# Optimization experiments

Hardware: AMD Instinct MI355X
Metric: run time of the kernel (lower is better)

The kernel has to match this reference:

```python
import jax, jax.numpy as jnp
import numpy as np

N_NODES = 50000
N_EDGES = 800000
C_FEAT = 96
HID = 96
C_CONST = 0.005


def _psi(v):
    return jnp.sign(v) * jnp.log(jnp.abs(v) + 1.0)


def setup_inputs() -> dict:
    key = jax.random.key(0)
    ks = jax.random.split(key, 16)
    d_e_in = 2 * C_FEAT + 2
    d_h_in = 2 * C_FEAT
    def w(k, fan_in, fan_out):
        return jax.random.normal(k, (fan_in, fan_out), jnp.float32) * (1.0 / np.sqrt(fan_in))
    return {
        "x": jax.random.normal(ks[0], (N_NODES, 4), jnp.float32),
        "h": jax.random.normal(ks[1], (N_NODES, C_FEAT), jnp.float32),
        "edge_i": jax.random.randint(ks[2], (N_EDGES,), 0, N_NODES, jnp.int32),
        "edge_j": jax.random.randint(ks[3], (N_EDGES,), 0, N_NODES, jnp.int32),
        "We1": w(ks[4], d_e_in, HID), "be1": jnp.zeros((HID,), jnp.float32),
        "We2": w(ks[5], HID, HID), "be2": jnp.zeros((HID,), jnp.float32),
        "Wm": w(ks[6], HID, 1), "bm": jnp.zeros((1,), jnp.float32),
        "Wh1": w(ks[7], d_h_in, HID), "bh1": jnp.zeros((HID,), jnp.float32),
        "Wh2": w(ks[8], HID, C_FEAT), "bh2": jnp.zeros((C_FEAT,), jnp.float32),
        "Wx1": w(ks[9], HID, HID), "bx1": jnp.zeros((HID,), jnp.float32),
        "Wx2": w(ks[10], HID, 1),  # bias-free last phi_x layer
    }


def reference(x, h, edge_i, edge_j, We1, be1, We2, be2, Wm, bm,
              Wh1, bh1, Wh2, bh2, Wx1, bx1, Wx2):
    n = x.shape[0]
    x_i = x[edge_i]            # (K,4)
    x_j = x[edge_j]            # (K,4)
    # Minkowski invariants: 2*t-component - full Euclidean sum == (+,-,-,-)
    d2 = jnp.square(x_i - x_j)
    norms = 2.0 * d2[..., 0] - jnp.sum(d2, axis=-1)
    z = x_i * x_j
    prods = 2.0 * z[..., 0] - jnp.sum(z, axis=-1)
    norms = _psi(norms)[:, None]   # (K,1)
    prods = _psi(prods)[:, None]   # (K,1)

    e_in = jnp.concatenate([h[edge_i], h[edge_j], norms, prods], axis=-1)  # (K,2C+2)
    m = jax.nn.relu(jax.nn.relu(e_in @ We1 + be1) @ We2 + be2)             # (K,HID)
    w_gate = jax.nn.sigmoid(m @ Wm + bm)                                   # (K,1)

    wm = jax.ops.segment_sum(w_gate * m, edge_i, num_segments=n)          # (N,HID)
    dh = jax.nn.relu(jnp.concatenate([h, wm], axis=-1) @ Wh1 + bh1) @ Wh2 + bh2
    h_out = h + dh

    phi_x = jax.nn.relu(m @ Wx1 + bx1) @ Wx2                              # (K,1)
    vals = phi_x * x_j                                                     # (K,4)
    s = jax.ops.segment_sum(vals, edge_i, num_segments=n)                 # (N,4)
    cnt = jax.ops.segment_sum(jnp.ones((vals.shape[0],), vals.dtype), edge_i, num_segments=n)
    mean = jnp.where(cnt[:, None] > 0, s / jnp.maximum(cnt[:, None], 1.0), 0.0)
    x_out = x + C_CONST * mean
    return (h_out, x_out)
```

## Files before the change

kernel.cpp:

```cpp
#include <hip/hip_runtime.h>
#include <math.h>

#define NN 50000
#define NE 800000
#define NB 196
#define TE 128

typedef __attribute__((ext_vector_type(8))) short short8v;
typedef __attribute__((ext_vector_type(4))) float f32x4;

__device__ __forceinline__ int rfl(int v) { return __builtin_amdgcn_readfirstlane(v); }
__device__ __forceinline__ unsigned short f2bf(float f) {
  unsigned u = __float_as_uint(f);
  u += 0x7FFFu + ((u >> 16) & 1u);
  return (unsigned short)(u >> 16);
}
__device__ __forceinline__ unsigned pk2(float a, float b) {
  return (unsigned)f2bf(a) | ((unsigned)f2bf(b) << 16);
}
__device__ __forceinline__ float bflo(unsigned u) { return __uint_as_float(u << 16); }
__device__ __forceinline__ float bfhi(unsigned u) { return __uint_as_float(u & 0xFFFF0000u); }

__global__ void khist(const int* __restrict__ ei, int* __restrict__ cnt) {
  const int i = blockIdx.x * 256 + threadIdx.x;
  atomicAdd(&cnt[ei[i]], 1);
}

__global__ void kscanA(const int* __restrict__ cnt, int* __restrict__ pre,
                       int* __restrict__ bsum) {
  __shared__ int ps[256];
  const int b = blockIdx.x, t = threadIdx.x, idx = b * 256 + t;
  const int v = (idx < NN) ? cnt[idx] : 0;
  ps[t] = v;
  __syncthreads();
  for (int off = 1; off < 256; off <<= 1) {
    const int u = (t >= off) ? ps[t - off] : 0;
    __syncthreads();
    ps[t] += u;
    __syncthreads();
  }
  if (idx < NN) pre[idx] = ps[t] - v;
  if (t == 255) bsum[b] = ps[255];
}

__global__ void kscanB(const int* __restrict__ bsum, int* __restrict__ boff) {
  __shared__ int ps[256];
  const int t = threadIdx.x;
  const int v = (t < NB) ? bsum[t] : 0;
  ps[t] = v;
  __syncthreads();
  for (int off = 1; off < 256; off <<= 1) {
    const int u = (t >= off) ? ps[t - off] : 0;
    __syncthreads();
    ps[t] += u;
    __syncthreads();
  }
  if (t < NB) boff[t] = ps[t] - v;
}

__global__ void kscanC(const int* __restrict__ pre, const int* __restrict__ boff,
                       int* __restrict__ base, int* __restrict__ cursor) {
  const int b = blockIdx.x, t = threadIdx.x, idx = b * 256 + t;
  if (idx < NN) {
    const int v = pre[idx] + boff[b];
    base[idx] = v;
    cursor[idx] = v;
  }
  if (idx == 0) base[NN] = NE;
}

__global__ void kperm(const int* __restrict__ ei, const int* __restrict__ ej,
                      int* __restrict__ cursor,
                      int* __restrict__ eis, int* __restrict__ ejs) {
  const int i = blockIdx.x * 256 + threadIdx.x;
  const int vi = ei[i];
  const int pos = atomicAdd(&cursor[vi], 1);
  eis[pos] = vi;
  ejs[pos] = ej[i];
}

__global__ void kwprep(const float* __restrict__ We1, const float* __restrict__ We2,
                       const float* __restrict__ Wx1, const float* __restrict__ Wh1,
                       const float* __restrict__ Wh2,
                       unsigned short* __restrict__ We1p, unsigned short* __restrict__ We2p,
                       unsigned short* __restrict__ Wx1p, unsigned short* __restrict__ Wh1p,
                       unsigned short* __restrict__ Wh2p) {
  const int t = blockIdx.x * 256 + threadIdx.x;
  const int j = t & 7, lane = (t >> 3) & 63;
  const int kk = (lane >> 4) * 8 + j;
  const int nn = lane & 15;
  {
    const int tile = t >> 9, tk = tile / 12, tn = tile % 12;
    const int k = tk * 32 + kk, n2 = tn * 16 + nn;
    const float v = (n2 < 96) ? We1[k * 96 + n2] : We1[(96 + k) * 96 + (n2 - 96)];
    We1p[t] = f2bf(v);
  }
  {
    const int tile = t >> 9, tk = tile / 6, tn = tile % 6;
    const int k = tk * 32 + kk, n = tn * 16 + nn;
    Wh1p[t] = f2bf(Wh1[k * 96 + n]);
  }
  if (t < 9216) {
    const int tile = t >> 9, tk = tile / 6, tn = tile % 6;
    const int k = tk * 32 + kk, n = tn * 16 + nn;
    We2p[t] = f2bf(We2[k * 96 + n]);
    Wx1p[t] = f2bf(Wx1[k * 96 + n]);
    Wh2p[t] = f2bf(Wh2[k * 96 + n]);
  }
}

__global__ __launch_bounds__(256, 4) void k0_AB(const float* __restrict__ h,
                                                const unsigned short* __restrict__ We1p,
                                                unsigned short* __restrict__ Abf,
                                                unsigned short* __restrict__ Bbf) {
  __shared__ __align__(16) unsigned short hbT[64 * 104];
  __shared__ __align__(16) unsigned short outT[64 * 200];
  const int tid = threadIdx.x;
  const int nb = blockIdx.x * 64;
  {
    const int e = tid & 63, q = tid >> 6;
    const int node = nb + e;
    const int nc = node < NN ? node : NN - 1;
    const float* hr = h + (long)nc * 96 + q * 24;
    unsigned* dst = (unsigned*)hbT + e * 52 + q * 12;
    #pragma unroll
    for (int c = 0; c < 6; ++c) {
      const float4 v = *(const float4*)(hr + c * 4);
      dst[c * 2]     = pk2(v.x, v.y);
      dst[c * 2 + 1] = pk2(v.z, v.w);
    }
  }
  __syncthreads();
  const int l = tid & 63, w = tid >> 6, cg = l & 15, rg = l >> 4;
  {
    const short8v* Wp = (const short8v*)We1p;
    const unsigned short* ar = hbT + (w * 16 + cg) * 104;
    const short8v af0 = *(const short8v*)(ar + rg * 8);
    const short8v af1 = *(const short8v*)(ar + 32 + rg * 8);
    const short8v af2 = *(const short8v*)(ar + 64 + rg * 8);
    #pragma unroll
    for (int tn = 0; tn < 12; ++tn) {
      f32x4 acc = (f32x4){0.f, 0.f, 0.f, 0.f};
      acc = __builtin_amdgcn_mfma_f32_16x16x32_bf16(af0, Wp[(0 * 12 + tn) * 64 + l], acc, 0, 0, 0);
      acc = __builtin_amdgcn_mfma_f32_16x16x32_bf16(af1, Wp[(1 * 12 + tn) * 64 + l], acc, 0, 0, 0);
      acc = __builtin_amdgcn_mfma_f32_16x16x32_bf16(af2, Wp[(2 * 12 + tn) * 64 + l], acc, 0, 0, 0);
      #pragma unroll
      for (int r = 0; r < 4; ++r)
        outT[(w * 16 + rg * 4 + r) * 200 + tn * 16 + cg] = f2bf(acc[r]);
    }
  }
  __syncthreads();
  {
    const int e = tid & 63, q = tid >> 6;
    const int node = nb + e;
    if (node < NN) {
      const unsigned* src = (const unsigned*)outT + e * 100;
      if (q < 2) {
        uint4* dA = (uint4*)(Abf + (size_t)node * 96);
        #pragma unroll
        for (int i = 0; i < 6; ++i) dA[q * 6 + i] = *(const uint4*)(src + (q * 6 + i) * 4);
      } else {
        uint4* dB = (uint4*)(Bbf + (size_t)node * 96);
        #pragma unroll
        for (int i = 0; i < 6; ++i) dB[(q - 2) * 6 + i] = *(const uint4*)(src + 48 + ((q - 2) * 6 + i) * 4);
      }
    }
  }
}

__global__ __launch_bounds__(256, 5) void k1_edge(const float* __restrict__ x,
    const unsigned short* __restrict__ Abf, const unsigned short* __restrict__ Bbf,
    const int* __restrict__ eis, const int* __restrict__ ejs,
    const float* __restrict__ We1, const float* __restrict__ be1,
    const unsigned short* __restrict__ We2p, const float* __restrict__ be2,
    const float* __restrict__ Wm, const float* __restrict__ bm,
    const unsigned short* __restrict__ Wx1p, const float* __restrict__ bx1,
    const float* __restrict__ Wx2,
    float* __restrict__ wmo, float* __restrict__ svo) {
  __shared__ __align__(16) unsigned short actT[TE * 104];
  __shared__ float gl[TE];
  __shared__ float phil[TE];
  __shared__ __align__(16) float xjl[TE * 4];
  __shared__ int vseq[TE + 2];
  __shared__ unsigned long long bmask[2];

  const int tid = threadIdx.x;
  const float bm0 = bm[0];
  const int tb = blockIdx.x * TE;

  {
    const int e2 = tid & 127, hf = tid >> 7;
    const int fb = hf * 48;
    const int vi = eis[tb + e2], vj = ejs[tb + e2];
    const float4 xi = *(const float4*)(x + (long)vi * 4);
    const float4 xj = *(const float4*)(x + (long)vj * 4);
    if (hf == 0) {
      vseq[1 + e2] = vi;
      *(float4*)(xjl + e2 * 4) = xj;
    }
    if (tid == 0) {
      vseq[0] = (tb > 0) ? eis[tb - 1] : -1;
      vseq[TE + 1] = (tb + TE < NE) ? eis[tb + TE] : -1;
    }
    const float d0 = xi.x - xj.x, d1 = xi.y - xj.y, d2 = xi.z - xj.z, d3 = xi.w - xj.w;
    const float nrm = d0 * d0 - d1 * d1 - d2 * d2 - d3 * d3;
    const float prd = xi.x * xj.x - xi.y * xj.y - xi.z * xj.z - xi.w * xj.w;
    const float pn = copysignf(logf(fabsf(nrm) + 1.f), nrm);
    const float pp = copysignf(logf(fabsf(prd) + 1.f), prd);
    const uint4* Ar = (const uint4*)(Abf + (size_t)vi * 96 + fb);
    const uint4* Br = (const uint4*)(Bbf + (size_t)vj * 96 + fb);
    const float* wA = We1 + 192 * 96 + fb;
    const float* wB = We1 + 193 * 96 + fb;
    const float* bE = be1 + fb;
    unsigned* arow = (unsigned*)actT + e2 * 52 + hf * 24;
    #pragma unroll
    for (int c = 0; c < 6; ++c) {
      const uint4 A4 = Ar[c], B4 = Br[c];
      const unsigned au[4] = {A4.x, A4.y, A4.z, A4.w};
      const unsigned bu[4] = {B4.x, B4.y, B4.z, B4.w};
      #pragma unroll
      for (int k2 = 0; k2 < 4; ++k2) {
        const int f = c * 8 + k2 * 2;
        const float lo = fmaxf(bflo(au[k2]) + bflo(bu[k2]) + pn * wA[f] + pp * wB[f] + bE[f], 0.f);
        const float hi = fmaxf(bfhi(au[k2]) + bfhi(bu[k2]) + pn * wA[f + 1] + pp * wB[f + 1] + bE[f + 1], 0.f);
        arow[c * 4 + k2] = pk2(lo, hi);
      }
    }
  }
  __syncthreads();

  if (tid < TE) {
    const int pred = (vseq[1 + tid] != vseq[2 + tid]) ? 1 : 0;
    const unsigned long long mk = __ballot(pred);
    if ((tid & 63) == 0) bmask[tid >> 6] = mk;
  }

  const int l = tid & 63, w = tid >> 6;
  const int cg = l & 15, rg = l >> 4;
  const int r0 = w * 32;
  const short8v* Wp2 = (const short8v*)We2p;
  const short8v* Wpx = (const short8v*)Wx1p;

  {
    short8v af[2][3];
    #pragma unroll
    for (int rt = 0; rt < 2; ++rt)
      #pragma unroll
      for (int tk = 0; tk < 3; ++tk)
        af[rt][tk] = *(const short8v*)(actT + (r0 + rt * 16 + cg) * 104 + tk * 32 + rg * 8);
    f32x4 acc[2][6];
    #pragma unroll
    for (int rt = 0; rt < 2; ++rt)
      #pragma unroll
      for (int tn = 0; tn < 6; ++tn) acc[rt][tn] = (f32x4){0.f, 0.f, 0.f, 0.f};
    #pragma unroll
    for (int tk = 0; tk < 3; ++tk)
      #pragma unroll
      for (int tn = 0; tn < 6; ++tn) {
        const short8v bf = Wp2[(tk * 6 + tn) * 64 + l];
        acc[0][tn] = __builtin_amdgcn_mfma_f32_16x16x32_bf16(af[0][tk], bf, acc[0][tn], 0, 0, 0);
        acc[1][tn] = __builtin_amdgcn_mfma_f32_16x16x32_bf16(af[1][tk], bf, acc[1][tn], 0, 0, 0);
      }
    #pragma unroll
    for (int rt = 0; rt < 2; ++rt) {
      float gp[4] = {0.f, 0.f, 0.f, 0.f};
      #pragma unroll
      for (int tn = 0; tn < 6; ++tn) {
        const int col = tn * 16 + cg;
        const float b = be2[col], wmw = Wm[col];
        #pragma unroll
        for (int r = 0; r < 4; ++r) {
          const float v = fmaxf(acc[rt][tn][r] + b, 0.f);
          gp[r] = fmaf(v, wmw, gp[r]);
          actT[(r0 + rt * 16 + rg * 4 + r) * 104 + col] = (unsigned short)f2bf(v);
        }
      }
      #pragma unroll
      for (int r = 0; r < 4; ++r) {
        float s = gp[r];
        s += __shfl_xor(s, 1); s += __shfl_xor(s, 2);
        s += __shfl_xor(s, 4); s += __shfl_xor(s, 8);
        if (cg == 0) gl[r0 + rt * 16 + rg * 4 + r] = 1.f / (1.f + expf(-(s + bm0)));
      }
    }
  }


  {
    short8v af[2][3];
    #pragma unroll
    for (int rt = 0; rt < 2; ++rt)
      #pragma unroll
      for (int tk = 0; tk < 3; ++tk)
        af[rt][tk] = *(const short8v*)(actT + (r0 + rt * 16 + cg) * 104 + tk * 32 + rg * 8);
    f32x4 acc[2][6];
    #pragma unroll
    for (int rt = 0; rt < 2; ++rt)
      #pragma unroll
      for (int tn = 0; tn < 6; ++tn) acc[rt][tn] = (f32x4){0.f, 0.f, 0.f, 0.f};
    #pragma unroll
    for (int tk = 0; tk < 3; ++tk)
      #pragma unroll
      for (int tn = 0; tn < 6; ++tn) {
        const short8v bf = Wpx[(tk * 6 + tn) * 64 + l];
        acc[0][tn] = __builtin_amdgcn_mfma_f32_16x16x32_bf16(af[0][tk], bf, acc[0][tn], 0, 0, 0);
        acc[1][tn] = __builtin_amdgcn_mfma_f32_16x16x32_bf16(af[1][tk], bf, acc[1][tn], 0, 0, 0);
      }
    #pragma unroll
    for (int rt = 0; rt < 2; ++rt) {
      float pp2[4] = {0.f, 0.f, 0.f, 0.f};
      #pragma unroll
      for (int tn = 0; tn < 6; ++tn) {
        const int col = tn * 16 + cg;
        const float b = bx1[col], wxw = Wx2[col];
        #pragma unroll
        for (int r = 0; r < 4; ++r)
          pp2[r] = fmaf(fmaxf(acc[rt][tn][r] + b, 0.f), wxw, pp2[r]);
      }
      #pragma unroll
      for (int r = 0; r < 4; ++r) {
        float s = pp2[r];
        s += __shfl_xor(s, 1); s += __shfl_xor(s, 2);
        s += __shfl_xor(s, 4); s += __shfl_xor(s, 8);
        if (cg == 0) phil[r0 + rt * 16 + rg * 4 + r] = s;
      }
    }
  }
  __syncthreads();

  if (tid < 192) {
    const int q0 = (tid >= 96) ? 1 : 0;
    const int col = tid - 96 * q0;
    #pragma unroll
    for (int pass = 0; pass < 2; ++pass) {
      const int q = q0 + 2 * pass;
      const int s_lo = q * 32;
      const unsigned long long mk = bmask[s_lo >> 6];
      float acc2 = 0.f;
      bool clean = (q == 0) ? (vseq[0] != vseq[1])
                            : (((bmask[(s_lo - 1) >> 6] >> ((s_lo - 1) & 63)) & 1ull) != 0);
      for (int i = 0; i < 32; ++i) {
        const int e = s_lo + i;
        acc2 = fmaf(gl[e], __uint_as_float(((unsigned)actT[e * 104 + col]) << 16), acc2);
        const bool gend = ((mk >> (e & 63)) & 1ull) != 0;
        if (gend || i == 31) {
          const int node = vseq[e + 1];
          float* dst = wmo + (size_t)node * 96 + col;
          if (clean && gend) *dst = acc2; else atomicAdd(dst, acc2);
          acc2 = 0.f; clean = true;
        }
      }
    }
  } else if (tid < 224) {
    const int t2 = tid - 192;
    const int comp = t2 & 3, q8 = t2 >> 2;
    const int s_lo = q8 * 16;
    const unsigned long long mk = bmask[s_lo >> 6];
    float acc2 = 0.f;
    bool clean = (q8 == 0) ? (vseq[0] != vseq[1])
                           : (((bmask[(s_lo - 1) >> 6] >> ((s_lo - 1) & 63)) & 1ull) != 0);
    for (int i = 0; i < 16; ++i) {
      const int e = s_lo + i;
      acc2 = fmaf(phil[e], xjl[e * 4 + comp], acc2);
      const bool gend = ((mk >> (e & 63)) & 1ull) != 0;
      if (gend || i == 15) {
        const int node = vseq[e + 1];
        float* dst = svo + (size_t)node * 4 + comp;
        if (clean && gend) *dst = acc2; else atomicAdd(dst, acc2);
        acc2 = 0.f; clean = true;
      }
    }
  }
}

__global__ __launch_bounds__(256, 4) void k3ab(const float* __restrict__ h,
    const float* __restrict__ wmv,
    const unsigned short* __restrict__ Wh1p, const float* __restrict__ bh1,
    const unsigned short* __restrict__ Wh2p, const float* __restrict__ bh2,
    const float* __restrict__ x, const float* __restrict__ svm,
    const int* __restrict__ basep,
    float* __restrict__ hout, float* __restrict__ xout) {
  __shared__ __align__(16) unsigned short inT[64 * 200];
  __shared__ __align__(16) unsigned short tmpT[64 * 104];
  const int tid = threadIdx.x;
  const int nb = blockIdx.x * 64;
  {
    const int e = tid & 63, q = tid >> 6;
    const int node = nb + e;
    const int nc = node < NN ? node : NN - 1;
    const float* hr = h + (long)nc * 96 + q * 24;
    const float* wr = wmv + (long)nc * 96 + q * 24;
    unsigned* dh = (unsigned*)inT + e * 100 + q * 12;
    unsigned* dw = (unsigned*)inT + e * 100 + 48 + q * 12;
    #pragma unroll
    for (int c = 0; c < 6; ++c) {
      const float4 v = *(const float4*)(hr + c * 4);
      dh[c * 2]     = pk2(v.x, v.y);
      dh[c * 2 + 1] = pk2(v.z, v.w);
      const float4 u = *(const float4*)(wr + c * 4);
      dw[c * 2]     = pk2(u.x, u.y);
      dw[c * 2 + 1] = pk2(u.z, u.w);
    }
  }
  __syncthreads();
  const int l = tid & 63, w = tid >> 6, cg = l & 15, rg = l >> 4;
  {
    const unsigned short* ar = inT + (w * 16 + cg) * 200;
    short8v af[6];
    #pragma unroll
    for (int tk = 0; tk < 6; ++tk) af[tk] = *(const short8v*)(ar + tk * 32 + rg * 8);
    const short8v* Wp = (const short8v*)Wh1p;
    #pragma unroll
    for (int tn = 0; tn < 6; ++tn) {
      f32x4 acc = (f32x4){0.f, 0.f, 0.f, 0.f};
      #pragma unroll
      for (int tk = 0; tk < 6; ++tk)
        acc = __builtin_amdgcn_mfma_f32_16x16x32_bf16(af[tk], Wp[(tk * 6 + tn) * 64 + l], acc, 0, 0, 0);
      const int col = tn * 16 + cg;
      const float b = bh1[col];
      #pragma unroll
      for (int r = 0; r < 4; ++r)
        tmpT[(w * 16 + rg * 4 + r) * 104 + col] = f2bf(fmaxf(acc[r] + b, 0.f));
    }
  }
  __syncthreads();
  {
    float* oT = (float*)inT;
    const unsigned short* mr = tmpT + (w * 16 + cg) * 104;
    const short8v mf0 = *(const short8v*)(mr + rg * 8);
    const short8v mf1 = *(const short8v*)(mr + 32 + rg * 8);
    const short8v mf2 = *(const short8v*)(mr + 64 + rg * 8);
    const short8v* Wp = (const short8v*)Wh2p;
    #pragma unroll
    for (int tn = 0; tn < 6; ++tn) {
      f32x4 acc = (f32x4){0.f, 0.f, 0.f, 0.f};
      acc = __builtin_amdgcn_mfma_f32_16x16x32_bf16(mf0, Wp[(0 * 6 + tn) * 64 + l], acc, 0, 0, 0);
      acc = __builtin_amdgcn_mfma_f32_16x16x32_bf16(mf1, Wp[(1 * 6 + tn) * 64 + l], acc, 0, 0, 0);
      acc = __builtin_amdgcn_mfma_f32_16x16x32_bf16(mf2, Wp[(2 * 6 + tn) * 64 + l], acc, 0, 0, 0);
      const int col = tn * 16 + cg;
      const float b = bh2[col];
      #pragma unroll
      for (int r = 0; r < 4; ++r)
        oT[(w * 16 + rg * 4 + r) * 100 + col] = acc[r] + b;
    }
  }
  __syncthreads();
  {
    const int e = tid & 63, q = tid >> 6;
    const int node = nb + e;
    if (node < NN) {
      const float* src = (const float*)inT + e * 100 + q * 24;
      const float* hr = h + (size_t)node * 96 + q * 24;
      float* dst = hout + (size_t)node * 96 + q * 24;
      #pragma unroll
      for (int c = 0; c < 6; ++c) {
        const float4 s = *(const float4*)(src + c * 4);
        const float4 hv = *(const float4*)(hr + c * 4);
        *(float4*)(dst + c * 4) = make_float4(hv.x + s.x, hv.y + s.y, hv.z + s.z, hv.w + s.w);
      }
    }
  }
  if (tid < 64) {
    const int node = nb + tid;
    if (node < NN) {
      const int cnt = basep[node + 1] - basep[node];
      const float inv = cnt > 0 ? 1.f / (float)cnt : 0.f;
      const float4 s4 = *(const float4*)(svm + (long)node * 4);
      const float4 xv = *(const float4*)(x + (long)node * 4);
      *(float4*)(xout + (long)node * 4) =
          make_float4(xv.x + 0.005f * s4.x * inv, xv.y + 0.005f * s4.y * inv,
                      xv.z + 0.005f * s4.z * inv, xv.w + 0.005f * s4.w * inv);
    }
  }
}

extern "C" void kernel_launch(void* const* d_in, const int* in_sizes, int n_in,
                              void* d_out, int out_size, void* d_ws, size_t ws_size,
                              hipStream_t stream) {
  const float* x   = (const float*)d_in[0];
  const float* h   = (const float*)d_in[1];
  const int*   ei  = (const int*)d_in[2];
  const int*   ej  = (const int*)d_in[3];
  const float* We1 = (const float*)d_in[4];
  const float* be1 = (const float*)d_in[5];
  const float* We2 = (const float*)d_in[6];
  const float* be2 = (const float*)d_in[7];
  const float* Wm  = (const float*)d_in[8];
  const float* bm  = (const float*)d_in[9];
  const float* Wh1 = (const float*)d_in[10];
  const float* bh1 = (const float*)d_in[11];
  const float* Wh2 = (const float*)d_in[12];
  const float* bh2 = (const float*)d_in[13];
  const float* Wx1 = (const float*)d_in[14];
  const float* bx1 = (const float*)d_in[15];
  const float* Wx2 = (const float*)d_in[16];

  char* w = (char*)d_ws;
  unsigned short* Abf  = (unsigned short*)w;
  unsigned short* Bbf  = (unsigned short*)(w + 9600000);
  float* WMv  = (float*)(w + 19200000);
  float* SvM  = (float*)(w + 38400000);
  int*   cnt  = (int*)(w + 39200000);
  int*   base = (int*)(w + 39400000);
  int*   curs = (int*)(w + 39600064);
  unsigned short* We2p = (unsigned short*)(w + 39800064);
  unsigned short* Wx1p = (unsigned short*)(w + 39818496);
  unsigned short* We1p = (unsigned short*)(w + 39836928);
  unsigned short* Wh1p = (unsigned short*)(w + 39873792);
  unsigned short* Wh2p = (unsigned short*)(w + 39910656);
  int*   eis  = (int*)(w + 39929088);
  int*   ejs  = (int*)(w + 43129088);
  int*   pre  = (int*)(w + 46329088);
  int*   bsum = (int*)(w + 46529088);
  int*   boff = (int*)(w + 46529872);

  float* hout = (float*)d_out;
  float* xout = hout + 4800000;

  hipMemsetAsync(cnt, 0, NN * sizeof(int), stream);
  hipMemsetAsync(WMv, 0, (size_t)(4800000 + 200000) * sizeof(float), stream);
  khist<<<NE / 256, 256, 0, stream>>>(ei, cnt);
  kscanA<<<NB, 256, 0, stream>>>(cnt, pre, bsum);
  kscanB<<<1, 256, 0, stream>>>(bsum, boff);
  kscanC<<<NB, 256, 0, stream>>>(pre, boff, base, curs);
  kperm<<<NE / 256, 256, 0, stream>>>(ei, ej, curs, eis, ejs);
  kwprep<<<72, 256, 0, stream>>>(We1, We2, Wx1, Wh1, Wh2, We1p, We2p, Wx1p, Wh1p, Wh2p);
  k0_AB<<<782, 256, 0, stream>>>(h, We1p, Abf, Bbf);
  k1_edge<<<NE / TE, 256, 0, stream>>>(x, Abf, Bbf, eis, ejs, We1, be1, We2p, be2,
                                       Wm, bm, Wx1p, bx1, Wx2, WMv, SvM);
  k3ab<<<782, 256, 0, stream>>>(h, WMv, Wh1p, bh1, Wh2p, bh2, x, SvM, base, hout, xout);
}
```

Baseline: 312.7 us.

## Fuse histogram with weight prep, load MFMA operands directly, tweak edge scatter

Merges the edge histogram and weight-packing kernels into one launch. k0_AB and k3ab now load h and wm straight from global memory into MFMA A-fragments instead of staging them through shared memory, which removes a barrier and LDS traffic and lets k0_AB raise its occupancy hint. It also adds s_setprio around MFMA loops, changes the activation LDS stride from 104 to 100, and rewrites the segmented scatter to walk whole segments using ctz on the boundary mask. The stride of 100 and the direct global loads may cause LDS bank conflicts or uncoalesced reads.

```diff
diff --git a/kernel.cpp b/kernel.cpp
--- a/kernel.cpp
+++ b/kernel.cpp
@@ -5,11 +5,11 @@
 #define NE 800000
 #define NB 196
 #define TE 128
+#define AST 100
 
 typedef __attribute__((ext_vector_type(8))) short short8v;
 typedef __attribute__((ext_vector_type(4))) float f32x4;
 
-__device__ __forceinline__ int rfl(int v) { return __builtin_amdgcn_readfirstlane(v); }
 __device__ __forceinline__ unsigned short f2bf(float f) {
   unsigned u = __float_as_uint(f);
   u += 0x7FFFu + ((u >> 16) & 1u);
@@ -20,10 +20,50 @@
 }
 __device__ __forceinline__ float bflo(unsigned u) { return __uint_as_float(u << 16); }
 __device__ __forceinline__ float bfhi(unsigned u) { return __uint_as_float(u & 0xFFFF0000u); }
-
-__global__ void khist(const int* __restrict__ ei, int* __restrict__ cnt) {
-  const int i = blockIdx.x * 256 + threadIdx.x;
-  atomicAdd(&cnt[ei[i]], 1);
+__device__ __forceinline__ short8v pack8(float4 a, float4 b) {
+  short8v r;
+  r[0] = (short)f2bf(a.x); r[1] = (short)f2bf(a.y);
+  r[2] = (short)f2bf(a.z); r[3] = (short)f2bf(a.w);
+  r[4] = (short)f2bf(b.x); r[5] = (short)f2bf(b.y);
+  r[6] = (short)f2bf(b.z); r[7] = (short)f2bf(b.w);
+  return r;
+}
+
+__global__ void kprep(const int* __restrict__ ei, int* __restrict__ cnt,
+                      const float* __restrict__ We1, const float* __restrict__ We2,
+                      const float* __restrict__ Wx1, const float* __restrict__ Wh1,
+                      const float* __restrict__ Wh2,
+                      unsigned short* __restrict__ We1p, unsigned short* __restrict__ We2p,
+                      unsigned short* __restrict__ Wx1p, unsigned short* __restrict__ Wh1p,
+                      unsigned short* __restrict__ Wh2p) {
+  const int b = blockIdx.x;
+  if (b < NE / 256) {
+    const int i = b * 256 + threadIdx.x;
+    atomicAdd(&cnt[ei[i]], 1);
+    return;
+  }
+  const int t = (b - NE / 256) * 256 + threadIdx.x;
+  const int j = t & 7, lane = (t >> 3) & 63;
+  const int kk = (lane >> 4) * 8 + j;
+  const int nn = lane & 15;
+  {
+    const int tile = t >> 9, tk = tile / 12, tn = tile % 12;
+    const int k = tk * 32 + kk, n2 = tn * 16 + nn;
+    const float v = (n2 < 96) ? We1[k * 96 + n2] : We1[(96 + k) * 96 + (n2 - 96)];
+    We1p[t] = f2bf(v);
+  }
+  {
+    const int tile = t >> 9, tk = tile / 6, tn = tile % 6;
+    const int k = tk * 32 + kk, n = tn * 16 + nn;
+    Wh1p[t] = f2bf(Wh1[k * 96 + n]);
+  }
+  if (t < 9216) {
+    const int tile = t >> 9, tk = tile / 6, tn = tile % 6;
+    const int k = tk * 32 + kk, n = tn * 16 + nn;
+    We2p[t] = f2bf(We2[k * 96 + n]);
+    Wx1p[t] = f2bf(Wx1[k * 96 + n]);
+    Wh2p[t] = f2bf(Wh2[k * 96 + n]);
+  }
 }
 
 __global__ void kscanA(const int* __restrict__ cnt, int* __restrict__ pre,
@@ -79,75 +119,36 @@
   ejs[pos] = ej[i];
 }
 
-__global__ void kwprep(const float* __restrict__ We1, const float* __restrict__ We2,
-                       const float* __restrict__ Wx1, const float* __restrict__ Wh1,
-                       const float* __restrict__ Wh2,
-                       unsigned short* __restrict__ We1p, unsigned short* __restrict__ We2p,
-                       unsigned short* __restrict__ Wx1p, unsigned short* __restrict__ Wh1p,
-                       unsigned short* __restrict__ Wh2p) {
-  const int t = blockIdx.x * 256 + threadIdx.x;
-  const int j = t & 7, lane = (t >> 3) & 63;
-  const int kk = (lane >> 4) * 8 + j;
-  const int nn = lane & 15;
-  {
-    const int tile = t >> 9, tk = tile / 12, tn = tile % 12;
-    const int k = tk * 32 + kk, n2 = tn * 16 + nn;
-    const float v = (n2 < 96) ? We1[k * 96 + n2] : We1[(96 + k) * 96 + (n2 - 96)];
-    We1p[t] = f2bf(v);
-  }
-  {
-    const int tile = t >> 9, tk = tile / 6, tn = tile % 6;
-    const int k = tk * 32 + kk, n = tn * 16 + nn;
-    Wh1p[t] = f2bf(Wh1[k * 96 + n]);
-  }
-  if (t < 9216) {
-    const int tile = t >> 9, tk = tile / 6, tn = tile % 6;
-    const int k = tk * 32 + kk, n = tn * 16 + nn;
-    We2p[t] = f2bf(We2[k * 96 + n]);
-    Wx1p[t] = f2bf(Wx1[k * 96 + n]);
-    Wh2p[t] = f2bf(Wh2[k * 96 + n]);
-  }
-}
-
-__global__ __launch_bounds__(256, 4) void k0_AB(const float* __restrict__ h,
+__global__ __launch_bounds__(256, 6) void k0_AB(const float* __restrict__ h,
                                                 const unsigned short* __restrict__ We1p,
                                                 unsigned short* __restrict__ Abf,
                                                 unsigned short* __restrict__ Bbf) {
-  __shared__ __align__(16) unsigned short hbT[64 * 104];
   __shared__ __align__(16) unsigned short outT[64 * 200];
   const int tid = threadIdx.x;
   const int nb = blockIdx.x * 64;
-  {
-    const int e = tid & 63, q = tid >> 6;
-    const int node = nb + e;
+  const int l = tid & 63, w = tid >> 6, cg = l & 15, rg = l >> 4;
+  {
+    const int node = nb + w * 16 + cg;
     const int nc = node < NN ? node : NN - 1;
-    const float* hr = h + (long)nc * 96 + q * 24;
-    unsigned* dst = (unsigned*)hbT + e * 52 + q * 12;
-    #pragma unroll
-    for (int c = 0; c < 6; ++c) {
-      const float4 v = *(const float4*)(hr + c * 4);
-      dst[c * 2]     = pk2(v.x, v.y);
-      dst[c * 2 + 1] = pk2(v.z, v.w);
-    }
-  }
-  __syncthreads();
-  const int l = tid & 63, w = tid >> 6, cg = l & 15, rg = l >> 4;
-  {
+    short8v af[3];
+    #pragma unroll
+    for (int tk = 0; tk < 3; ++tk) {
+      const float* p = h + (size_t)nc * 96 + tk * 32 + rg * 8;
+      af[tk] = pack8(*(const float4*)p, *(const float4*)(p + 4));
+    }
     const short8v* Wp = (const short8v*)We1p;
-    const unsigned short* ar = hbT + (w * 16 + cg) * 104;
-    const short8v af0 = *(const short8v*)(ar + rg * 8);
-    const short8v af1 = *(const short8v*)(ar + 32 + rg * 8);
-    const short8v af2 = *(const short8v*)(ar + 64 + rg * 8);
+    __builtin_amdgcn_s_setprio(1);
     #pragma unroll
     for (int tn = 0; tn < 12; ++tn) {
       f32x4 acc = (f32x4){0.f, 0.f, 0.f, 0.f};
-      acc = __builtin_amdgcn_mfma_f32_16x16x32_bf16(af0, Wp[(0 * 12 + tn) * 64 + l], acc, 0, 0, 0);
-      acc = __builtin_amdgcn_mfma_f32_16x16x32_bf16(af1, Wp[(1 * 12 + tn) * 64 + l], acc, 0, 0, 0);
-      acc = __builtin_amdgcn_mfma_f32_16x16x32_bf16(af2, Wp[(2 * 12 + tn) * 64 + l], acc, 0, 0, 0);
+      acc = __builtin_amdgcn_mfma_f32_16x16x32_bf16(af[0], Wp[(0 * 12 + tn) * 64 + l], acc, 0, 0, 0);
+      acc = __builtin_amdgcn_mfma_f32_16x16x32_bf16(af[1], Wp[(1 * 12 + tn) * 64 + l], acc, 0, 0, 0);
+      acc = __builtin_amdgcn_mfma_f32_16x16x32_bf16(af[2], Wp[(2 * 12 + tn) * 64 + l], acc, 0, 0, 0);
       #pragma unroll
       for (int r = 0; r < 4; ++r)
         outT[(w * 16 + rg * 4 + r) * 200 + tn * 16 + cg] = f2bf(acc[r]);
     }
+    __builtin_amdgcn_s_setprio(0);
   }
   __syncthreads();
   {
@@ -177,7 +178,7 @@
     const unsigned short* __restrict__ Wx1p, const float* __restrict__ bx1,
     const float* __restrict__ Wx2,
     float* __restrict__ wmo, float* __restrict__ svo) {
-  __shared__ __align__(16) unsigned short actT[TE * 104];
+  __shared__ __align__(16) unsigned short actT[TE * AST];
   __shared__ float gl[TE];
   __shared__ float phil[TE];
   __shared__ __align__(16) float xjl[TE * 4];
@@ -212,7 +213,7 @@
     const float* wA = We1 + 192 * 96 + fb;
     const float* wB = We1 + 193 * 96 + fb;
     const float* bE = be1 + fb;
-    unsigned* arow = (unsigned*)actT + e2 * 52 + hf * 24;
+    unsigned* arow = (unsigned*)actT + e2 * (AST / 2) + hf * 24;
     #pragma unroll
     for (int c = 0; c < 6; ++c) {
       const uint4 A4 = Ar[c], B4 = Br[c];
@@ -247,12 +248,13 @@
     for (int rt = 0; rt < 2; ++rt)
       #pragma unroll
       for (int tk = 0; tk < 3; ++tk)
-        af[rt][tk] = *(const short8v*)(actT + (r0 + rt * 16 + cg) * 104 + tk * 32 + rg * 8);
+        af[rt][tk] = *(const short8v*)(actT + (r0 + rt * 16 + cg) * AST + tk * 32 + rg * 8);
     f32x4 acc[2][6];
     #pragma unroll
     for (int rt = 0; rt < 2; ++rt)
       #pragma unroll
       for (int tn = 0; tn < 6; ++tn) acc[rt][tn] = (f32x4){0.f, 0.f, 0.f, 0.f};
+    __builtin_amdgcn_s_setprio(1);
     #pragma unroll
     for (int tk = 0; tk < 3; ++tk)
       #pragma unroll
@@ -261,6 +263,7 @@
         acc[0][tn] = __builtin_amdgcn_mfma_f32_16x16x32_bf16(af[0][tk], bf, acc[0][tn], 0, 0, 0);
         acc[1][tn] = __builtin_amdgcn_mfma_f32_16x16x32_bf16(af[1][tk], bf, acc[1][tn], 0, 0, 0);
       }
+    __builtin_amdgcn_s_setprio(0);
     #pragma unroll
     for (int rt = 0; rt < 2; ++rt) {
       float gp[4] = {0.f, 0.f, 0.f, 0.f};
@@ -272,7 +275,7 @@
         for (int r = 0; r < 4; ++r) {
           const float v = fmaxf(acc[rt][tn][r] + b, 0.f);
           gp[r] = fmaf(v, wmw, gp[r]);
-          actT[(r0 + rt * 16 + rg * 4 + r) * 104 + col] = (unsigned short)f2bf(v);
+          actT[(r0 + rt * 16 + rg * 4 + r) * AST + col] = (unsigned short)f2bf(v);
         }
       }
       #pragma unroll
@@ -292,12 +295,13 @@
     for (int rt = 0; rt < 2; ++rt)
       #pragma unroll
       for (int tk = 0; tk < 3; ++tk)
-        af[rt][tk] = *(const short8v*)(actT + (r0 + rt * 16 + cg) * 104 + tk * 32 + rg * 8);
+        af[rt][tk] = *(const short8v*)(actT + (r0 + rt * 16 + cg) * AST + tk * 32 + rg * 8);
     f32x4 acc[2][6];
     #pragma unroll
     for (int rt = 0; rt < 2; ++rt)
       #pragma unroll
       for (int tn = 0; tn < 6; ++tn) acc[rt][tn] = (f32x4){0.f, 0.f, 0.f, 0.f};
+    __builtin_amdgcn_s_setprio(1);
     #pragma unroll
     for (int tk = 0; tk < 3; ++tk)
       #pragma unroll
@@ -306,6 +310,7 @@
         acc[0][tn] = __builtin_amdgcn_mfma_f32_16x16x32_bf16(af[0][tk], bf, acc[0][tn], 0, 0, 0);
         acc[1][tn] = __builtin_amdgcn_mfma_f32_16x16x32_bf16(af[1][tk], bf, acc[1][tn], 0, 0, 0);
       }
+    __builtin_amdgcn_s_setprio(0);
     #pragma unroll
     for (int rt = 0; rt < 2; ++rt) {
       float pp2[4] = {0.f, 0.f, 0.f, 0.f};
@@ -334,41 +339,49 @@
     #pragma unroll
     for (int pass = 0; pass < 2; ++pass) {
       const int q = q0 + 2 * pass;
-      const int s_lo = q * 32;
-      const unsigned long long mk = bmask[s_lo >> 6];
+      const int s_lo = q * 32, s_hi = s_lo + 32;
+      const unsigned long long mk = bmask[q >> 1];
       float acc2 = 0.f;
       bool clean = (q == 0) ? (vseq[0] != vseq[1])
                             : (((bmask[(s_lo - 1) >> 6] >> ((s_lo - 1) & 63)) & 1ull) != 0);
-      for (int i = 0; i < 32; ++i) {
-        const int e = s_lo + i;
-        acc2 = fmaf(gl[e], __uint_as_float(((unsigned)actT[e * 104 + col]) << 16), acc2);
-        const bool gend = ((mk >> (e & 63)) & 1ull) != 0;
-        if (gend || i == 31) {
-          const int node = vseq[e + 1];
-          float* dst = wmo + (size_t)node * 96 + col;
-          if (clean && gend) *dst = acc2; else atomicAdd(dst, acc2);
-          acc2 = 0.f; clean = true;
-        }
+      int e = s_lo;
+      while (e < s_hi) {
+        const unsigned long long rem = mk >> (e & 63);
+        const int span = rem ? (int)__builtin_ctzll(rem) : 64;
+        int end = e + span;
+        const bool gend = (end < s_hi);
+        if (end > s_hi - 1) end = s_hi - 1;
+        for (int i = e; i <= end; ++i)
+          acc2 = fmaf(gl[i], __uint_as_float(((unsigned)actT[i * AST + col]) << 16), acc2);
+        const int node = vseq[end + 1];
+        float* dst = wmo + (size_t)node * 96 + col;
+        if (clean && gend) *dst = acc2; else atomicAdd(dst, acc2);
+        acc2 = 0.f; clean = true;
+        e = end + 1;
       }
     }
   } else if (tid < 224) {
     const int t2 = tid - 192;
     const int comp = t2 & 3, q8 = t2 >> 2;
-    const int s_lo = q8 * 16;
-    const unsigned long long mk = bmask[s_lo >> 6];
+    const int s_lo = q8 * 16, s_hi = s_lo + 16;
+    const unsigned long long mk = bmask[q8 >> 2];
     float acc2 = 0.f;
     bool clean = (q8 == 0) ? (vseq[0] != vseq[1])
                            : (((bmask[(s_lo - 1) >> 6] >> ((s_lo - 1) & 63)) & 1ull) != 0);
-    for (int i = 0; i < 16; ++i) {
-      const int e = s_lo + i;
-      acc2 = fmaf(phil[e], xjl[e * 4 + comp], acc2);
-      const bool gend = ((mk >> (e & 63)) & 1ull) != 0;
-      if (gend || i == 15) {
-        const int node = vseq[e + 1];
-        float* dst = svo + (size_t)node * 4 + comp;
-        if (clean && gend) *dst = acc2; else atomicAdd(dst, acc2);
-        acc2 = 0.f; clean = true;
-      }
+    int e = s_lo;
+    while (e < s_hi) {
+      const unsigned long long rem = mk >> (e & 63);
+      const int span = rem ? (int)__builtin_ctzll(rem) : 64;
+      int end = e + span;
+      const bool gend = (end < s_hi);
+      if (end > s_hi - 1) end = s_hi - 1;
+      for (int i = e; i <= end; ++i)
+        acc2 = fmaf(phil[i], xjl[i * 4 + comp], acc2);
+      const int node = vseq[end + 1];
+      float* dst = svo + (size_t)node * 4 + comp;
+      if (clean && gend) *dst = acc2; else atomicAdd(dst, acc2);
+      acc2 = 0.f; clean = true;
+      e = end + 1;
     }
   }
 }
@@ -380,36 +393,24 @@
     const float* __restrict__ x, const float* __restrict__ svm,
     const int* __restrict__ basep,
     float* __restrict__ hout, float* __restrict__ xout) {
-  __shared__ __align__(16) unsigned short inT[64 * 200];
   __shared__ __align__(16) unsigned short tmpT[64 * 104];
+  __shared__ __align__(16) float oT[64 * 100];
   const int tid = threadIdx.x;
   const int nb = blockIdx.x * 64;
-  {
-    const int e = tid & 63, q = tid >> 6;
-    const int node = nb + e;
+  const int l = tid & 63, w = tid >> 6, cg = l & 15, rg = l >> 4;
+  {
+    const int node = nb + w * 16 + cg;
     const int nc = node < NN ? node : NN - 1;
-    const float* hr = h + (long)nc * 96 + q * 24;
-    const float* wr = wmv + (long)nc * 96 + q * 24;
-    unsigned* dh = (unsigned*)inT + e * 100 + q * 12;
-    unsigned* dw = (unsigned*)inT + e * 100 + 48 + q * 12;
-    #pragma unroll
-    for (int c = 0; c < 6; ++c) {
-      const float4 v = *(const float4*)(hr + c * 4);
-      dh[c * 2]     = pk2(v.x, v.y);
-      dh[c * 2 + 1] = pk2(v.z, v.w);
-      const float4 u = *(const float4*)(wr + c * 4);
-      dw[c * 2]     = pk2(u.x, u.y);
-      dw[c * 2 + 1] = pk2(u.z, u.w);
-    }
-  }
-  __syncthreads();
-  const int l = tid & 63, w = tid >> 6, cg = l & 15, rg = l >> 4;
-  {
-    const unsigned short* ar = inT + (w * 16 + cg) * 200;
     short8v af[6];
     #pragma unroll
-    for (int tk = 0; tk < 6; ++tk) af[tk] = *(const short8v*)(ar + tk * 32 + rg * 8);
+    for (int tk = 0; tk < 3; ++tk) {
+      const float* p = h + (size_t)nc * 96 + tk * 32 + rg * 8;
+      af[tk] = pack8(*(const float4*)p, *(const float4*)(p + 4));
+      const float* pw = wmv + (size_t)nc * 96 + tk * 32 + rg * 8;
+      af[3 + tk] = pack8(*(const float4*)pw, *(const float4*)(pw + 4));
+    }
     const short8v* Wp = (const short8v*)Wh1p;
+    __builtin_amdgcn_s_setprio(1);
     #pragma unroll
     for (int tn = 0; tn < 6; ++tn) {
       f32x4 acc = (f32x4){0.f, 0.f, 0.f, 0.f};
@@ -422,15 +423,15 @@
       for (int r = 0; r < 4; ++r)
         tmpT[(w * 16 + rg * 4 + r) * 104 + col] = f2bf(fmaxf(acc[r] + b, 0.f));
     }
-  }
-  __syncthreads();
-  {
-    float* oT = (float*)inT;
+    __builtin_amdgcn_s_setprio(0);
+  }
+  {
     const unsigned short* mr = tmpT + (w * 16 + cg) * 104;
     const short8v mf0 = *(const short8v*)(mr + rg * 8);
     const short8v mf1 = *(const short8v*)(mr + 32 + rg * 8);
     const short8v mf2 = *(const short8v*)(mr + 64 + rg * 8);
     const short8v* Wp = (const short8v*)Wh2p;
+    __builtin_amdgcn_s_setprio(1);
     #pragma unroll
     for (int tn = 0; tn < 6; ++tn) {
       f32x4 acc = (f32x4){0.f, 0.f, 0.f, 0.f};
@@ -443,13 +444,14 @@
       for (int r = 0; r < 4; ++r)
         oT[(w * 16 + rg * 4 + r) * 100 + col] = acc[r] + b;
     }
+    __builtin_amdgcn_s_setprio(0);
   }
   __syncthreads();
   {
     const int e = tid & 63, q = tid >> 6;
     const int node = nb + e;
     if (node < NN) {
-      const float* src = (const float*)inT + e * 100 + q * 24;
+      const float* src = oT + e * 100 + q * 24;
       const float* hr = h + (size_t)node * 96 + q * 24;
       float* dst = hout + (size_t)node * 96 + q * 24;
       #pragma unroll
@@ -519,12 +521,12 @@
 
   hipMemsetAsync(cnt, 0, NN * sizeof(int), stream);
   hipMemsetAsync(WMv, 0, (size_t)(4800000 + 200000) * sizeof(float), stream);
-  khist<<<NE / 256, 256, 0, stream>>>(ei, cnt);
+  kprep<<<NE / 256 + 72, 256, 0, stream>>>(ei, cnt, We1, We2, Wx1, Wh1, Wh2,
+                                           We1p, We2p, Wx1p, Wh1p, Wh2p);
   kscanA<<<NB, 256, 0, stream>>>(cnt, pre, bsum);
   kscanB<<<1, 256, 0, stream>>>(bsum, boff);
   kscanC<<<NB, 256, 0, stream>>>(pre, boff, base, curs);
   kperm<<<NE / 256, 256, 0, stream>>>(ei, ej, curs, eis, ejs);
-  kwprep<<<72, 256, 0, stream>>>(We1, We2, Wx1, Wh1, Wh2, We1p, We2p, Wx1p, Wh1p, Wh2p);
   k0_AB<<<782, 256, 0, stream>>>(h, We1p, Abf, Bbf);
   k1_edge<<<NE / TE, 256, 0, stream>>>(x, Abf, Bbf, eis, ejs, We1, be1, We2p, be2,
                                        Wm, bm, Wx1p, bx1, Wx2, WMv, SvM);
```

New measurement: 317.8 us. About the same (+1.6%).
